# Optimization experiments

Measured on AMD Instinct MI355X. Metric: run time of the kernel, lower is better.

The kernel has to match this reference:

```python
import jax, jax.numpy as jnp
import numpy as np

HIDDEN_DIM = 32
EDGE_DIM = 16
EDGE_HIDDEN = 64
N_EDGES = 250000


def setup_inputs() -> dict:
    key = jax.random.key(0)
    k1, k2, k3, k4, k5 = jax.random.split(key, 5)
    h_v = jax.random.normal(k1, (N_EDGES, HIDDEN_DIM), dtype=jnp.float32)
    h_w = jax.random.normal(k2, (N_EDGES, HIDDEN_DIM), dtype=jnp.float32)
    edge_features = jax.random.normal(k3, (N_EDGES, EDGE_DIM), dtype=jnp.float32)
    # Edge-network MLP params: edge_dim -> edge_hidden -> hidden_dim^2
    W1 = jax.random.normal(k4, (EDGE_DIM, EDGE_HIDDEN), dtype=jnp.float32) * (1.0 / np.sqrt(EDGE_DIM))
    b1 = jnp.zeros((EDGE_HIDDEN,), dtype=jnp.float32)
    W2 = jax.random.normal(k5, (EDGE_HIDDEN, HIDDEN_DIM * HIDDEN_DIM), dtype=jnp.float32) * (1.0 / np.sqrt(EDGE_HIDDEN))
    b2 = jnp.zeros((HIDDEN_DIM * HIDDEN_DIM,), dtype=jnp.float32)
    return {"h_v": h_v, "h_w": h_w, "edge_features": edge_features,
            "W1": W1, "b1": b1, "W2": W2, "b2": b2}


def reference(h_v, h_w, edge_features, W1, b1, W2, b2):
    # 1. Edge MLP: (n_edges, edge_dim) -> (n_edges, d*d)
    hdn = jax.nn.relu(edge_features @ W1 + b1)          # (E, edge_hidden)
    A = (hdn @ W2 + b2)                                  # (E, d*d)
    # 2. Reshape to per-edge matrices (E, d, d)
    d = h_w.shape[-1]
    A = A.reshape(-1, d, d)
    # 3. Per-edge matrix-vector product: M = A(e_vw) @ h_w
    messages = jnp.einsum('eij,ej->ei', A, h_w)          # (E, d)
    return messages
```

## Files before the change

### kernel.cpp

```cpp
#include <hip/hip_runtime.h>

typedef unsigned short u16;
typedef _Float16 f16x2 __attribute__((ext_vector_type(2)));
typedef _Float16 f16x8 __attribute__((ext_vector_type(8)));
typedef float    f32x4  __attribute__((ext_vector_type(4)));
typedef float    f32x16 __attribute__((ext_vector_type(16)));


union U4 { uint4 u; f16x8 h; u16 s[8]; };
union HU { f16x2 h2[4]; f16x8 h8; };

__global__ void prep_kernel(const float* __restrict__ W1,
                            const float* __restrict__ b1,
                            const float* __restrict__ W2,
                            const float* __restrict__ b2,
                            u16* __restrict__ ws)
{
    int id = blockIdx.x * 256 + threadIdx.x;
    if (id < 8320) {
        int k2 = id >> 6, l = id & 63;
        int h = l >> 5, col = l & 31;
        U4 o;
        #pragma unroll
        for (int g = 0; g < 2; ++g) {
            int base4 = k2 * 16 + g * 8 + h * 4;
            f32x4 v;
            if (base4 < 2048) {
                int k1 = base4 >> 5, j32 = base4 & 31;
                v = *(const f32x4*)&W2[k1 * 1024 + col * 32 + j32];
            } else {
                v = *(const f32x4*)&b2[col * 32 + (base4 - 2048)];
            }
            #pragma unroll
            for (int j = 0; j < 4; ++j)
                o.h[g * 4 + j] = (_Float16)v[j];
        }
        *(uint4*)(ws + id * 8) = o.u;
    } else if (id < 8448) {
        int idx = id - 8320;
        int nt = idx >> 6, l = idx & 63;
        int h = l >> 5, col = nt * 32 + (l & 31);
        U4 o;
        #pragma unroll
        for (int g = 0; g < 2; ++g)
            #pragma unroll
            for (int j = 0; j < 4; ++j) {
                int k = g * 8 + h * 4 + j;
                o.h[g * 4 + j] = (_Float16)W1[k * 64 + col];
            }
        *(uint4*)(ws + id * 8) = o.u;
    } else if (id < 8512) {
        int idx = id - 8448;
        int hh = idx >> 5, nt = (idx >> 4) & 1, r = idx & 15;
        int row = (r & 3) + 8 * (r >> 2) + 4 * hh;
        ((float*)(ws + 67584))[idx] = b1[nt * 32 + row];
    }
}

__device__ __forceinline__ void stage16(const void* g, void* l) {
    __builtin_amdgcn_global_load_lds(
        (const __attribute__((address_space(1))) void*)g,
        (__attribute__((address_space(3))) void*)l, 16, 0, 0);
}

__global__ __launch_bounds__(256, 3) void edge_kernel(
    const float* __restrict__ h_w,
    const float* __restrict__ ef,
    const u16*  __restrict__ ws,
    float* __restrict__ out,
    int E)
{
    __shared__ alignas(16) u16 shm[16384];
    const int tid  = threadIdx.x;
    const int lane = tid & 63;
    const int l31  = lane & 31;
    const int h    = lane >> 5;
    const int tileBase = (blockIdx.x * 4 + (tid >> 6)) * 64;
    const char* wsb = (const char*)ws;
    char*       shb = (char*)shm;

    #pragma unroll
    for (int j = 0; j < 4; ++j)
        stage16(wsb + j * 4096 + tid * 16, shb + j * 4096 + tid * 16);

    f16x2 hwA[2][2][4];
    #pragma unroll
    for (int mt = 0; mt < 2; ++mt) {
        int e = tileBase + mt * 32 + l31;
        bool ok = e < E;
        f32x4 q0 = {}, q1 = {}, q2 = {}, q3 = {};
        if (ok) {
            const float* hp = h_w + (size_t)e * 32 + h * 4;
            q0 = *(const f32x4*)(hp);
            q1 = *(const f32x4*)(hp + 8);
            q2 = *(const f32x4*)(hp + 16);
            q3 = *(const f32x4*)(hp + 24);
        }
        hwA[mt][0][0] = f16x2{ (_Float16)q0[0], (_Float16)q0[1] };
        hwA[mt][0][1] = f16x2{ (_Float16)q0[2], (_Float16)q0[3] };
        hwA[mt][0][2] = f16x2{ (_Float16)q1[0], (_Float16)q1[1] };
        hwA[mt][0][3] = f16x2{ (_Float16)q1[2], (_Float16)q1[3] };
        hwA[mt][1][0] = f16x2{ (_Float16)q2[0], (_Float16)q2[1] };
        hwA[mt][1][1] = f16x2{ (_Float16)q2[2], (_Float16)q2[3] };
        hwA[mt][1][2] = f16x2{ (_Float16)q3[0], (_Float16)q3[1] };
        hwA[mt][1][3] = f16x2{ (_Float16)q3[2], (_Float16)q3[3] };
    }

    const uint4* W1f = (const uint4*)(ws + 8320 * 8);
    U4 w1f0, w1f1;
    w1f0.u = W1f[lane];
    w1f1.u = W1f[64 + lane];
    const float* b1pf = (const float*)(ws + 67584);
    f32x4 bv[2][4];
    #pragma unroll
    for (int nt = 0; nt < 2; ++nt)
        #pragma unroll
        for (int qr = 0; qr < 4; ++qr)
            bv[nt][qr] = *(const f32x4*)(b1pf + h * 32 + nt * 16 + qr * 4);

    f16x2 Q[2][2][8][2];
    #pragma unroll
    for (int mt = 0; mt < 2; ++mt) {
        int e = tileBase + mt * 32 + l31;
        bool ok = e < E;
        f32x4 g0 = {}, g1 = {};
        if (ok) {
            g0 = *(const f32x4*)&ef[e * 16 + h * 4];
            g1 = *(const f32x4*)&ef[e * 16 + 8 + h * 4];
        }
        U4 a;
        #pragma unroll
        for (int j = 0; j < 4; ++j) {
            a.h[j]     = (_Float16)g0[j];
            a.h[4 + j] = (_Float16)g1[j];
        }
        f32x16 c0 = {}, c1 = {};
        c0 = __builtin_amdgcn_mfma_f32_32x32x16_f16(w1f0.h, a.h, c0, 0, 0, 0);
        c1 = __builtin_amdgcn_mfma_f32_32x32x16_f16(w1f1.h, a.h, c1, 0, 0, 0);
        #pragma unroll
        for (int nt = 0; nt < 2; ++nt) {
            #pragma unroll
            for (int p = 0; p < 8; ++p) {
                float r0 = (nt ? c1[2 * p]     : c0[2 * p]);
                float r1 = (nt ? c1[2 * p + 1] : c0[2 * p + 1]);
                float v0 = fmaxf(r0 + bv[nt][p >> 1][(2 * p) & 3],     0.f);
                float v1 = fmaxf(r1 + bv[nt][p >> 1][(2 * p + 1) & 3], 0.f);
                f16x2 own = { (_Float16)v0, (_Float16)v1 };
                unsigned swu = __shfl_xor(__builtin_bit_cast(unsigned, own), 32, 64);
                f16x2 sw = __builtin_bit_cast(f16x2, swu);
                Q[mt][nt][p][0] = h ? sw : own;
                Q[mt][nt][p][1] = h ? own : sw;
            }
        }
    }

    f32x16 acc0 = {}, acc1 = {};
    __syncthreads();

    #pragma unroll
    for (int c = 0; c < 8; ++c) {
        if (c < 7) {
            #pragma unroll
            for (int j = 0; j < 4; ++j)
                stage16(wsb + (c + 1) * 16384 + j * 4096 + tid * 16,
                        shb + ((c + 1) & 1) * 16384 + j * 4096 + tid * 16);
        } else {
            if (tid < 128)
                stage16(wsb + 131072 + tid * 16, shb + tid * 16);
        }
        const char* bB = shb + (c & 1) * 16384;
        #pragma unroll
        for (int qq = 0; qq < 8; ++qq) {
            const int k1   = c * 8 + qq;
            const int nt   = k1 >> 5;
            const int q    = k1 & 31;
            const int pa   = ((q & 3) >> 1) + 2 * (q >> 3);
            const int half = q & 1;
            const int hq   = (q >> 2) & 1;
            U4 bf0, bf1;
            bf0.u = *(const uint4*)(bB + (2 * qq) * 1024 + lane * 16);
            bf1.u = *(const uint4*)(bB + (2 * qq + 1) * 1024 + lane * 16);
            _Float16 x0 = Q[0][nt][pa][hq][half];
            _Float16 x1 = Q[1][nt][pa][hq][half];
            f16x2 hh0 = { x0, x0 }, hh1 = { x1, x1 };
            HU A0, A1;
            #pragma unroll
            for (int rr = 0; rr < 4; ++rr) { A0.h2[rr] = hh0 * hwA[0][0][rr]; A1.h2[rr] = hh1 * hwA[1][0][rr]; }
            acc0 = __builtin_amdgcn_mfma_f32_32x32x16_f16(A0.h8, bf0.h, acc0, 0, 0, 0);
            acc1 = __builtin_amdgcn_mfma_f32_32x32x16_f16(A1.h8, bf0.h, acc1, 0, 0, 0);
            #pragma unroll
            for (int rr = 0; rr < 4; ++rr) { A0.h2[rr] = hh0 * hwA[0][1][rr]; A1.h2[rr] = hh1 * hwA[1][1][rr]; }
            acc0 = __builtin_amdgcn_mfma_f32_32x32x16_f16(A0.h8, bf1.h, acc0, 0, 0, 0);
            acc1 = __builtin_amdgcn_mfma_f32_32x32x16_f16(A1.h8, bf1.h, acc1, 0, 0, 0);
        }
        __syncthreads();
    }

    {
        U4 bf0, bf1;
        bf0.u = *(const uint4*)(shb + lane * 16);
        bf1.u = *(const uint4*)(shb + 1024 + lane * 16);
        HU A0, A1;
        #pragma unroll
        for (int rr = 0; rr < 4; ++rr) { A0.h2[rr] = hwA[0][0][rr]; A1.h2[rr] = hwA[1][0][rr]; }
        acc0 = __builtin_amdgcn_mfma_f32_32x32x16_f16(A0.h8, bf0.h, acc0, 0, 0, 0);
        acc1 = __builtin_amdgcn_mfma_f32_32x32x16_f16(A1.h8, bf0.h, acc1, 0, 0, 0);
        #pragma unroll
        for (int rr = 0; rr < 4; ++rr) { A0.h2[rr] = hwA[0][1][rr]; A1.h2[rr] = hwA[1][1][rr]; }
        acc0 = __builtin_amdgcn_mfma_f32_32x32x16_f16(A0.h8, bf1.h, acc0, 0, 0, 0);
        acc1 = __builtin_amdgcn_mfma_f32_32x32x16_f16(A1.h8, bf1.h, acc1, 0, 0, 0);
    }

    #pragma unroll
    for (int mt = 0; mt < 2; ++mt) {
        #pragma unroll
        for (int r = 0; r < 16; ++r) {
            int row = (r & 3) + 8 * (r >> 2) + 4 * h;
            int e = tileBase + mt * 32 + row;
            float v = (mt == 0) ? acc0[r] : acc1[r];
            if (e < E) out[(size_t)e * 32 + l31] = v;
        }
    }
}

extern "C" void kernel_launch(void* const* d_in, const int* in_sizes, int n_in,
                              void* d_out, int out_size, void* d_ws, size_t ws_size,
                              hipStream_t stream)
{
    const float* h_w = (const float*)d_in[1];
    const float* ef  = (const float*)d_in[2];
    const float* W1  = (const float*)d_in[3];
    const float* b1  = (const float*)d_in[4];
    const float* W2  = (const float*)d_in[5];
    const float* b2  = (const float*)d_in[6];
    float* out = (float*)d_out;
    const int E = in_sizes[1] / 32;
    u16* ws = (u16*)d_ws;

    prep_kernel<<<34, 256, 0, stream>>>(W1, b1, W2, b2, ws);

    const int blocks = (E + 255) / 256;
    edge_kernel<<<blocks, 256, 0, stream>>>(h_w, ef, ws, out, E);
}
```

Measured before the change: 47.25 us.

## Process four 32-edge tiles per wave and replace cross-lane shuffle with swapped W1 MFMA

Each wave now handles 128 edges (four M-tiles) instead of 64, so every W2 fragment read from LDS feeds four MFMAs instead of two, and half as many blocks each stage the full W2 stream. The shfl_xor exchange of the hidden activations is replaced by a second pair of MFMAs against a column-swapped copy of W1, built in the prep kernel, so each lane computes both halves directly. The LDS B-fragment reads are software-prefetched one step ahead. In exchange, register pressure rises sharply (launch bounds drop to 2 blocks per SM), first-layer MFMA work doubles, and fewer blocks give less latency hiding.

```diff
diff --git a/kernel.cpp b/kernel.cpp
--- a/kernel.cpp
+++ b/kernel.cpp
@@ -36,10 +36,13 @@
                 o.h[g * 4 + j] = (_Float16)v[j];
         }
         *(uint4*)(ws + id * 8) = o.u;
-    } else if (id < 8448) {
+    } else if (id < 8576) {
         int idx = id - 8320;
-        int nt = idx >> 6, l = idx & 63;
-        int h = l >> 5, col = nt * 32 + (l & 31);
+        int sw  = idx >> 7;
+        int nt = (idx >> 6) & 1, l = idx & 63;
+        int h = l >> 5;
+        int c31 = sw ? ((l & 31) ^ 4) : (l & 31);
+        int col = nt * 32 + c31;
         U4 o;
         #pragma unroll
         for (int g = 0; g < 2; ++g)
@@ -49,11 +52,11 @@
                 o.h[g * 4 + j] = (_Float16)W1[k * 64 + col];
             }
         *(uint4*)(ws + id * 8) = o.u;
-    } else if (id < 8512) {
-        int idx = id - 8448;
+    } else if (id < 8640) {
+        int idx = id - 8576;
         int hh = idx >> 5, nt = (idx >> 4) & 1, r = idx & 15;
         int row = (r & 3) + 8 * (r >> 2) + 4 * hh;
-        ((float*)(ws + 67584))[idx] = b1[nt * 32 + row];
+        ((float*)(ws + 68608))[idx] = b1[nt * 32 + row];
     }
 }
 
@@ -63,7 +66,7 @@
         (__attribute__((address_space(3))) void*)l, 16, 0, 0);
 }
 
-__global__ __launch_bounds__(256, 3) void edge_kernel(
+__global__ __launch_bounds__(256, 2) void edge_kernel(
     const float* __restrict__ h_w,
     const float* __restrict__ ef,
     const u16*  __restrict__ ws,
@@ -75,7 +78,7 @@
     const int lane = tid & 63;
     const int l31  = lane & 31;
     const int h    = lane >> 5;
-    const int tileBase = (blockIdx.x * 4 + (tid >> 6)) * 64;
+    const int tileBase = (blockIdx.x * 4 + (tid >> 6)) * 128;
     const char* wsb = (const char*)ws;
     char*       shb = (char*)shm;
 
@@ -83,9 +86,9 @@
     for (int j = 0; j < 4; ++j)
         stage16(wsb + j * 4096 + tid * 16, shb + j * 4096 + tid * 16);
 
-    f16x2 hwA[2][2][4];
-    #pragma unroll
-    for (int mt = 0; mt < 2; ++mt) {
+    f16x2 hwA[4][2][4];
+    #pragma unroll
+    for (int mt = 0; mt < 4; ++mt) {
         int e = tileBase + mt * 32 + l31;
         bool ok = e < E;
         f32x4 q0 = {}, q1 = {}, q2 = {}, q3 = {};
@@ -106,21 +109,24 @@
         hwA[mt][1][3] = f16x2{ (_Float16)q3[2], (_Float16)q3[3] };
     }
 
-    const uint4* W1f = (const uint4*)(ws + 8320 * 8);
-    U4 w1f0, w1f1;
-    w1f0.u = W1f[lane];
-    w1f1.u = W1f[64 + lane];
-    const float* b1pf = (const float*)(ws + 67584);
-    f32x4 bv[2][4];
+    const uint4* W1f  = (const uint4*)(ws + 66560);
+    const uint4* W1fs = (const uint4*)(ws + 67584);
+    U4 wn0, wn1, wsw0, wsw1;
+    wn0.u  = W1f[lane];   wn1.u  = W1f[64 + lane];
+    wsw0.u = W1fs[lane];  wsw1.u = W1fs[64 + lane];
+    const float* b1pf = (const float*)(ws + 68608);
+    f32x4 bvo[2][4], bvf[2][4];
     #pragma unroll
     for (int nt = 0; nt < 2; ++nt)
         #pragma unroll
-        for (int qr = 0; qr < 4; ++qr)
-            bv[nt][qr] = *(const f32x4*)(b1pf + h * 32 + nt * 16 + qr * 4);
-
-    f16x2 Q[2][2][8][2];
-    #pragma unroll
-    for (int mt = 0; mt < 2; ++mt) {
+        for (int qr = 0; qr < 4; ++qr) {
+            bvo[nt][qr] = *(const f32x4*)(b1pf + h * 32 + nt * 16 + qr * 4);
+            bvf[nt][qr] = *(const f32x4*)(b1pf + (1 - h) * 32 + nt * 16 + qr * 4);
+        }
+
+    f16x2 QA[4][2][8], QB[4][2][8];
+    #pragma unroll
+    for (int mt = 0; mt < 4; ++mt) {
         int e = tileBase + mt * 32 + l31;
         bool ok = e < E;
         f32x4 g0 = {}, g1 = {};
@@ -134,27 +140,29 @@
             a.h[j]     = (_Float16)g0[j];
             a.h[4 + j] = (_Float16)g1[j];
         }
-        f32x16 c0 = {}, c1 = {};
-        c0 = __builtin_amdgcn_mfma_f32_32x32x16_f16(w1f0.h, a.h, c0, 0, 0, 0);
-        c1 = __builtin_amdgcn_mfma_f32_32x32x16_f16(w1f1.h, a.h, c1, 0, 0, 0);
+        f32x16 cn0 = {}, cn1 = {}, cs0 = {}, cs1 = {};
+        cn0 = __builtin_amdgcn_mfma_f32_32x32x16_f16(wn0.h,  a.h, cn0, 0, 0, 0);
+        cn1 = __builtin_amdgcn_mfma_f32_32x32x16_f16(wn1.h,  a.h, cn1, 0, 0, 0);
+        cs0 = __builtin_amdgcn_mfma_f32_32x32x16_f16(wsw0.h, a.h, cs0, 0, 0, 0);
+        cs1 = __builtin_amdgcn_mfma_f32_32x32x16_f16(wsw1.h, a.h, cs1, 0, 0, 0);
         #pragma unroll
         for (int nt = 0; nt < 2; ++nt) {
             #pragma unroll
             for (int p = 0; p < 8; ++p) {
-                float r0 = (nt ? c1[2 * p]     : c0[2 * p]);
-                float r1 = (nt ? c1[2 * p + 1] : c0[2 * p + 1]);
-                float v0 = fmaxf(r0 + bv[nt][p >> 1][(2 * p) & 3],     0.f);
-                float v1 = fmaxf(r1 + bv[nt][p >> 1][(2 * p + 1) & 3], 0.f);
-                f16x2 own = { (_Float16)v0, (_Float16)v1 };
-                unsigned swu = __shfl_xor(__builtin_bit_cast(unsigned, own), 32, 64);
-                f16x2 sw = __builtin_bit_cast(f16x2, swu);
-                Q[mt][nt][p][0] = h ? sw : own;
-                Q[mt][nt][p][1] = h ? own : sw;
-            }
-        }
-    }
-
-    f32x16 acc0 = {}, acc1 = {};
+                const int r0 = 2 * p, r1 = 2 * p + 1;
+                float n0 = fmaxf((nt ? cn1[r0] : cn0[r0]) + bvo[nt][r0 >> 2][r0 & 3], 0.f);
+                float n1 = fmaxf((nt ? cn1[r1] : cn0[r1]) + bvo[nt][r1 >> 2][r1 & 3], 0.f);
+                float s0 = fmaxf((nt ? cs1[r0] : cs0[r0]) + bvf[nt][r0 >> 2][r0 & 3], 0.f);
+                float s1 = fmaxf((nt ? cs1[r1] : cs0[r1]) + bvf[nt][r1 >> 2][r1 & 3], 0.f);
+                f16x2 pn = { (_Float16)n0, (_Float16)n1 };
+                f16x2 ps = { (_Float16)s0, (_Float16)s1 };
+                QA[mt][nt][p] = h ? ps : pn;
+                QB[mt][nt][p] = h ? pn : ps;
+            }
+        }
+    }
+
+    f32x16 acc[4] = {};
     __syncthreads();
 
     #pragma unroll
@@ -169,29 +177,34 @@
                 stage16(wsb + 131072 + tid * 16, shb + tid * 16);
         }
         const char* bB = shb + (c & 1) * 16384;
+        U4 cur0, cur1, nxt0, nxt1;
+        cur0.u = *(const uint4*)(bB + lane * 16);
+        cur1.u = *(const uint4*)(bB + 1024 + lane * 16);
         #pragma unroll
         for (int qq = 0; qq < 8; ++qq) {
+            if (qq < 7) {
+                nxt0.u = *(const uint4*)(bB + (2 * qq + 2) * 1024 + lane * 16);
+                nxt1.u = *(const uint4*)(bB + (2 * qq + 3) * 1024 + lane * 16);
+            }
             const int k1   = c * 8 + qq;
             const int nt   = k1 >> 5;
-            const int q    = k1 & 31;
-            const int pa   = ((q & 3) >> 1) + 2 * (q >> 3);
-            const int half = q & 1;
-            const int hq   = (q >> 2) & 1;
-            U4 bf0, bf1;
-            bf0.u = *(const uint4*)(bB + (2 * qq) * 1024 + lane * 16);
-            bf1.u = *(const uint4*)(bB + (2 * qq + 1) * 1024 + lane * 16);
-            _Float16 x0 = Q[0][nt][pa][hq][half];
-            _Float16 x1 = Q[1][nt][pa][hq][half];
-            f16x2 hh0 = { x0, x0 }, hh1 = { x1, x1 };
-            HU A0, A1;
-            #pragma unroll
-            for (int rr = 0; rr < 4; ++rr) { A0.h2[rr] = hh0 * hwA[0][0][rr]; A1.h2[rr] = hh1 * hwA[1][0][rr]; }
-            acc0 = __builtin_amdgcn_mfma_f32_32x32x16_f16(A0.h8, bf0.h, acc0, 0, 0, 0);
-            acc1 = __builtin_amdgcn_mfma_f32_32x32x16_f16(A1.h8, bf0.h, acc1, 0, 0, 0);
-            #pragma unroll
-            for (int rr = 0; rr < 4; ++rr) { A0.h2[rr] = hh0 * hwA[0][1][rr]; A1.h2[rr] = hh1 * hwA[1][1][rr]; }
-            acc0 = __builtin_amdgcn_mfma_f32_32x32x16_f16(A0.h8, bf1.h, acc0, 0, 0, 0);
-            acc1 = __builtin_amdgcn_mfma_f32_32x32x16_f16(A1.h8, bf1.h, acc1, 0, 0, 0);
+            const int kk   = k1 & 31;
+            const int hq   = (kk >> 2) & 1;
+            const int p    = ((kk >> 3) << 1) + ((kk & 3) >> 1);
+            const int half = kk & 1;
+            #pragma unroll
+            for (int mt = 0; mt < 4; ++mt) {
+                _Float16 x = hq ? QB[mt][nt][p][half] : QA[mt][nt][p][half];
+                f16x2 hh = { x, x };
+                HU A;
+                #pragma unroll
+                for (int rr = 0; rr < 4; ++rr) A.h2[rr] = hh * hwA[mt][0][rr];
+                acc[mt] = __builtin_amdgcn_mfma_f32_32x32x16_f16(A.h8, cur0.h, acc[mt], 0, 0, 0);
+                #pragma unroll
+                for (int rr = 0; rr < 4; ++rr) A.h2[rr] = hh * hwA[mt][1][rr];
+                acc[mt] = __builtin_amdgcn_mfma_f32_32x32x16_f16(A.h8, cur1.h, acc[mt], 0, 0, 0);
+            }
+            if (qq < 7) { cur0 = nxt0; cur1 = nxt1; }
         }
         __syncthreads();
     }
@@ -200,25 +213,25 @@
         U4 bf0, bf1;
         bf0.u = *(const uint4*)(shb + lane * 16);
         bf1.u = *(const uint4*)(shb + 1024 + lane * 16);
-        HU A0, A1;
-        #pragma unroll
-        for (int rr = 0; rr < 4; ++rr) { A0.h2[rr] = hwA[0][0][rr]; A1.h2[rr] = hwA[1][0][rr]; }
-        acc0 = __builtin_amdgcn_mfma_f32_32x32x16_f16(A0.h8, bf0.h, acc0, 0, 0, 0);
-        acc1 = __builtin_amdgcn_mfma_f32_32x32x16_f16(A1.h8, bf0.h, acc1, 0, 0, 0);
-        #pragma unroll
-        for (int rr = 0; rr < 4; ++rr) { A0.h2[rr] = hwA[0][1][rr]; A1.h2[rr] = hwA[1][1][rr]; }
-        acc0 = __builtin_amdgcn_mfma_f32_32x32x16_f16(A0.h8, bf1.h, acc0, 0, 0, 0);
-        acc1 = __builtin_amdgcn_mfma_f32_32x32x16_f16(A1.h8, bf1.h, acc1, 0, 0, 0);
-    }
-
-    #pragma unroll
-    for (int mt = 0; mt < 2; ++mt) {
+        #pragma unroll
+        for (int mt = 0; mt < 4; ++mt) {
+            HU A;
+            #pragma unroll
+            for (int rr = 0; rr < 4; ++rr) A.h2[rr] = hwA[mt][0][rr];
+            acc[mt] = __builtin_amdgcn_mfma_f32_32x32x16_f16(A.h8, bf0.h, acc[mt], 0, 0, 0);
+            #pragma unroll
+            for (int rr = 0; rr < 4; ++rr) A.h2[rr] = hwA[mt][1][rr];
+            acc[mt] = __builtin_amdgcn_mfma_f32_32x32x16_f16(A.h8, bf1.h, acc[mt], 0, 0, 0);
+        }
+    }
+
+    #pragma unroll
+    for (int mt = 0; mt < 4; ++mt) {
         #pragma unroll
         for (int r = 0; r < 16; ++r) {
             int row = (r & 3) + 8 * (r >> 2) + 4 * h;
             int e = tileBase + mt * 32 + row;
-            float v = (mt == 0) ? acc0[r] : acc1[r];
-            if (e < E) out[(size_t)e * 32 + l31] = v;
+            if (e < E) out[(size_t)e * 32 + l31] = acc[mt][r];
         }
     }
 }
@@ -239,6 +252,6 @@
 
     prep_kernel<<<34, 256, 0, stream>>>(W1, b1, W2, b2, ws);
 
-    const int blocks = (E + 255) / 256;
+    const int blocks = (E + 511) / 512;
     edge_kernel<<<blocks, 256, 0, stream>>>(h_w, ef, ws, out, E);
 }
```

Measured after the change: 77.85 us. +64.8%, slower.
